# Kernel tuning notes

Measured on AMD Instinct MI355X. Metric: run time of the kernel, lower is better.

## Reference

```python
import jax, jax.numpy as jnp
import numpy as np

THRESH = 0.1        # Huber threshold (self.threshold)
CORR_WT = 1.0       # corr_wt
ENTROPY_WT = 0.0001 # entropy_wt
BS, N = 32, 1024    # n_pts = nv = 1024 hardcoded in multi_pose_with_pts


def setup_inputs() -> dict:
    key = jax.random.key(0)
    ks = jax.random.split(key, 7)
    return {
        "points_1": jax.random.normal(ks[0], (BS, N, 3), jnp.float32),
        "points_2": jax.random.normal(ks[1], (BS, N, 3), jnp.float32),
        "assign_mat_1": jax.random.normal(ks[2], (BS, N, N), jnp.float32),
        "assign_mat_2": jax.random.normal(ks[3], (BS, N, N), jnp.float32),
        "scale": jax.random.uniform(ks[4], (BS,), jnp.float32, 0.5, 1.5),
        "rotation": jax.random.normal(ks[5], (BS, 3, 3), jnp.float32),
        "translation": jax.random.normal(ks[6], (BS, 3), jnp.float32),
    }


def _transform(sRt, pts):
    # apply 4x4 pose to [b, n, 3] points (homogeneous, keep xyz)
    return jnp.einsum('bij,bnj->bni', sRt[:, :3, :3], pts) + sRt[:, :3, 3][:, None, :]


def _chamfer(x, y):
    # squared pairwise distances [b, n, m]; loss = mean min both directions
    d = (jnp.sum(x * x, -1)[:, :, None] + jnp.sum(y * y, -1)[:, None, :]
         - 2.0 * jnp.einsum('bnd,bmd->bnm', x, y))
    d = jnp.maximum(d, 0.0)
    return jnp.mean(jnp.min(d, axis=2)) + jnp.mean(jnp.min(d, axis=1))


def _corr(a, b):
    # smooth-L1-like (Huber) correspondence loss
    diff = jnp.abs(a - b)
    loss = jnp.where(diff > THRESH, diff - THRESH / 2.0, diff * diff / (2.0 * THRESH))
    return CORR_WT * jnp.mean(jnp.sum(loss, axis=2))


def _entropy(assign_mat, soft_assign, axis):
    log_assign = jax.nn.log_softmax(assign_mat, axis=axis)
    return ENTROPY_WT * jnp.mean(-jnp.sum(soft_assign * log_assign, axis=axis))


def _cos_loss(m1, m2, eps=1e-8):
    a = m1.reshape(m1.shape[0], -1)
    b = m2.reshape(m2.shape[0], -1)
    na = jnp.maximum(jnp.linalg.norm(a, axis=1), eps)
    nb = jnp.maximum(jnp.linalg.norm(b, axis=1), eps)
    return jnp.mean(1.0 - jnp.sum(a * b, axis=1) / (na * nb))


def reference(points_1, points_2, assign_mat_1, assign_mat_2, scale, rotation, translation):
    sa1 = jax.nn.softmax(assign_mat_1, axis=2)
    sa2 = jax.nn.softmax(assign_mat_2, axis=2)

    # pose_dict_RT: sRt = [[s*R, t], [0, 1]]
    sR = rotation * scale[:, None, None]
    sRt = jnp.concatenate([sR, translation[:, :, None]], axis=2)          # b 3 4
    bottom = jnp.broadcast_to(jnp.array([0., 0., 0., 1.], sRt.dtype), (sRt.shape[0], 1, 4))
    sRt12 = jnp.concatenate([sRt, bottom], axis=1)                        # b 4 4
    sRt21 = jnp.linalg.inv(sRt12)

    p1in2 = jnp.einsum('bnm,bmd->bnd', sa1, points_2)
    p2in1 = jnp.einsum('bnm,bmd->bnd', sa2, points_1)
    p1to2 = _transform(sRt12, points_1)
    p2to1 = _transform(sRt21, points_2)

    cd1 = _chamfer(p1to2, p1in2)
    cd2 = _chamfer(p2to1, p2in1)
    total = (cd1 + cd2
             + _corr(p1in2, p1to2) + _corr(p2in1, p2to1)
             + _entropy(assign_mat_1, sa1, 2) + _entropy(assign_mat_2, sa2, 2)
             + _cos_loss(assign_mat_1, assign_mat_2)
             + _entropy(assign_mat_1, sa1, 1) + _entropy(assign_mat_2, sa2, 1))
    return total
```

## Files before the change

kernel.cpp:

```cpp
#include <hip/hip_runtime.h>
#include <math.h>

#define BSZ 32
#define NP  1024

#define OFF_ACC   0
#define OFF_COS   8
#define OFF_POSE  104
#define OFF_P1IN2 872
#define OFF_P2IN1 (OFF_P1IN2 + 98304)
#define OFF_INVR  (OFF_P2IN1 + 98304)
#define OFF_COLP  (OFF_INVR + 65536)

__global__ void k_pose(const float* __restrict__ scale,
                       const float* __restrict__ rot,
                       const float* __restrict__ tr,
                       float* __restrict__ ws) {
    int t = threadIdx.x;
    if (t < 52) {
        ws[OFF_ACC + 2 * t]     = 0.f;
        ws[OFF_ACC + 2 * t + 1] = 0.f;
    }
    if (t >= BSZ) return;
    int b = t;
    float s = scale[b];
    float M[9];
#pragma unroll
    for (int i = 0; i < 9; ++i) M[i] = rot[b * 9 + i] * s;
    float t0 = tr[b * 3 + 0], t1 = tr[b * 3 + 1], t2 = tr[b * 3 + 2];
    float det = M[0] * (M[4] * M[8] - M[5] * M[7])
              - M[1] * (M[3] * M[8] - M[5] * M[6])
              + M[2] * (M[3] * M[7] - M[4] * M[6]);
    float id = 1.0f / det;
    float inv[9];
    inv[0] =  (M[4] * M[8] - M[5] * M[7]) * id;
    inv[1] = -(M[1] * M[8] - M[2] * M[7]) * id;
    inv[2] =  (M[1] * M[5] - M[2] * M[4]) * id;
    inv[3] = -(M[3] * M[8] - M[5] * M[6]) * id;
    inv[4] =  (M[0] * M[8] - M[2] * M[6]) * id;
    inv[5] = -(M[0] * M[5] - M[2] * M[3]) * id;
    inv[6] =  (M[3] * M[7] - M[4] * M[6]) * id;
    inv[7] = -(M[0] * M[7] - M[1] * M[6]) * id;
    inv[8] =  (M[0] * M[4] - M[1] * M[3]) * id;
    float u0 = -(inv[0] * t0 + inv[1] * t1 + inv[2] * t2);
    float u1 = -(inv[3] * t0 + inv[4] * t1 + inv[5] * t2);
    float u2 = -(inv[6] * t0 + inv[7] * t1 + inv[8] * t2);
    float* P = ws + OFF_POSE + b * 24;
#pragma unroll
    for (int i = 0; i < 9; ++i) P[i] = M[i];
    P[9] = t0; P[10] = t1; P[11] = t2;
#pragma unroll
    for (int i = 0; i < 9; ++i) P[12 + i] = inv[i];
    P[21] = u0; P[22] = u1; P[23] = u2;
}

__global__ __launch_bounds__(256) void k_rows(
    const float* __restrict__ am1, const float* __restrict__ am2,
    const float* __restrict__ pts1, const float* __restrict__ pts2,
    float* __restrict__ p1in2, float* __restrict__ p2in1,
    float* __restrict__ invR, float* __restrict__ acc) {
    __shared__ float sred[8];
    const int bid = blockIdx.x;
    const int rb = bid & 31;
    const int m  = (bid >> 5) & 1;
    const int b  = bid >> 6;
    const int wv = threadIdx.x >> 6, ln = threadIdx.x & 63;
    const int row0 = rb * 32 + wv * 8;
    const float* am  = m ? am2 : am1;
    const float* pts = m ? pts1 : pts2;
    float* pout   = m ? p2in1 : p1in2;
    float* invout = invR + (m * BSZ + b) * NP;

    float P[16][3];
#pragma unroll
    for (int j = 0; j < 4; ++j)
#pragma unroll
        for (int k = 0; k < 4; ++k) {
            int c = 256 * j + 4 * ln + k;
            const float* p = pts + ((size_t)b * NP + c) * 3;
            P[4 * j + k][0] = p[0];
            P[4 * j + k][1] = p[1];
            P[4 * j + k][2] = p[2];
        }

    float e2a = 0.f, sSa = 0.f;
    const float4* rA = (const float4*)(am + ((size_t)b * NP + row0) * NP);

#pragma unroll 1
    for (int r = 0; r < 8; ++r) {
        float4 a[4];
#pragma unroll
        for (int j = 0; j < 4; ++j) a[j] = rA[(size_t)r * 256 + ln + 64 * j];
        float R = 0.f, Su = 0.f, q0 = 0.f, q1 = 0.f, q2 = 0.f;
#pragma unroll
        for (int j = 0; j < 4; ++j) {
            float* e = (float*)&a[j];
#pragma unroll
            for (int k = 0; k < 4; ++k) {
                int i = 4 * j + k;
                float v  = e[k];
                float ex = __expf(v);
                R += ex; Su += ex * v;
                q0 += ex * P[i][0]; q1 += ex * P[i][1]; q2 += ex * P[i][2];
            }
        }
#pragma unroll
        for (int s = 1; s < 64; s <<= 1) {
            R  += __shfl_xor(R, s);  Su += __shfl_xor(Su, s);
            q0 += __shfl_xor(q0, s); q1 += __shfl_xor(q1, s); q2 += __shfl_xor(q2, s);
        }
        if (ln == 0) {
            float inv = 1.0f / R;
            float S = Su * inv;
            e2a += __logf(R) - S;
            sSa += S;
            int row = row0 + r;
            invout[row] = inv;
            float* o = pout + ((size_t)b * NP + row) * 3;
            o[0] = q0 * inv; o[1] = q1 * inv; o[2] = q2 * inv;
        }
    }
    if (ln == 0) { sred[wv] = e2a; sred[4 + wv] = sSa; }
    __syncthreads();
    if (threadIdx.x == 0) {
        atomicAdd(&acc[0], sred[0] + sred[1] + sred[2] + sred[3]);
        atomicAdd(&acc[1], sred[4] + sred[5] + sred[6] + sred[7]);
    }
}

__global__ __launch_bounds__(256) void k_cols2(
    const float* __restrict__ am1, const float* __restrict__ am2,
    const float* __restrict__ invR, float* __restrict__ colP,
    float* __restrict__ cosacc) {
    __shared__ float invL[64];
    __shared__ float cred[12];
    const int rt = blockIdx.x & 31;
    const int b  = blockIdx.x >> 5;
    const int t  = threadIdx.x;
    if (t < 64) {
        int mm = t >> 5, rr = t & 31;
        invL[t] = invR[(mm * BSZ + b) * NP + rt * 32 + rr];
    }
    __syncthreads();
    const float4* s1 = (const float4*)(am1 + ((size_t)b * NP + rt * 32) * NP) + t;
    const float4* s2 = (const float4*)(am2 + ((size_t)b * NP + rt * 32) * NP) + t;
    float C1x=0,C1y=0,C1z=0,C1w=0, T1x=0,T1y=0,T1z=0,T1w=0;
    float C2x=0,C2y=0,C2z=0,C2w=0, T2x=0,T2y=0,T2z=0,T2w=0;
    float dacc = 0.f, n1a = 0.f, n2a = 0.f;
#pragma unroll 4
    for (int r = 0; r < 32; ++r) {
        float4 v1 = s1[(size_t)r * 256];
        float4 v2 = s2[(size_t)r * 256];
        dacc += v1.x*v2.x + v1.y*v2.y + v1.z*v2.z + v1.w*v2.w;
        n1a  += v1.x*v1.x + v1.y*v1.y + v1.z*v1.z + v1.w*v1.w;
        n2a  += v2.x*v2.x + v2.y*v2.y + v2.z*v2.z + v2.w*v2.w;
        float w1 = invL[r], w2 = invL[32 + r];
        float e;
        e = __expf(v1.x); C1x += e; T1x += e * w1;
        e = __expf(v1.y); C1y += e; T1y += e * w1;
        e = __expf(v1.z); C1z += e; T1z += e * w1;
        e = __expf(v1.w); C1w += e; T1w += e * w1;
        e = __expf(v2.x); C2x += e; T2x += e * w2;
        e = __expf(v2.y); C2y += e; T2y += e * w2;
        e = __expf(v2.z); C2z += e; T2z += e * w2;
        e = __expf(v2.w); C2w += e; T2w += e * w2;
    }
    float4* cp = (float4*)colP + ((size_t)(b * 32 + rt)) * 1024 + t;
    cp[0]   = make_float4(C1x, C1y, C1z, C1w);
    cp[256] = make_float4(T1x, T1y, T1z, T1w);
    cp[512] = make_float4(C2x, C2y, C2z, C2w);
    cp[768] = make_float4(T2x, T2y, T2z, T2w);
#pragma unroll
    for (int s = 1; s < 64; s <<= 1) {
        dacc += __shfl_xor(dacc, s);
        n1a  += __shfl_xor(n1a, s);
        n2a  += __shfl_xor(n2a, s);
    }
    if ((t & 63) == 0) {
        int wv = t >> 6;
        cred[wv] = dacc; cred[4 + wv] = n1a; cred[8 + wv] = n2a;
    }
    __syncthreads();
    if (t == 0) {
        atomicAdd(&cosacc[b],      cred[0] + cred[1] + cred[2]  + cred[3]);
        atomicAdd(&cosacc[32 + b], cred[4] + cred[5] + cred[6]  + cred[7]);
        atomicAdd(&cosacc[64 + b], cred[8] + cred[9] + cred[10] + cred[11]);
    }
}

__global__ void k_colred2(const float* __restrict__ colP, float* __restrict__ acc) {
    int idx = blockIdx.x * 256 + threadIdx.x;
    int bm = idx >> 10;
    int c  = idx & 1023;
    int b = bm >> 1, m = bm & 1;
    const float* base = colP + (size_t)b * 32 * 4 * NP + (2 * m) * NP + c;
    float C = 0.f, T = 0.f;
#pragma unroll
    for (int rt = 0; rt < 32; ++rt) {
        C += base[(size_t)rt * 4 * NP];
        T += base[(size_t)rt * 4 * NP + NP];
    }
    float v = T * __logf(C);
#pragma unroll
    for (int s = 1; s < 64; s <<= 1) v += __shfl_xor(v, s);
    if ((threadIdx.x & 63) == 0) atomicAdd(&acc[2], v);
}

__global__ __launch_bounds__(256) void k_cham(
    const float* __restrict__ p1, const float* __restrict__ p2,
    const float* __restrict__ p1in2, const float* __restrict__ p2in1,
    const float* __restrict__ pose, float* __restrict__ acc) {
    __shared__ float4 ys[NP];
    const int blk   = blockIdx.x;
    const int chunk = blk & 3;
    const int b     = (blk >> 2) & 31;
    const int dir   = (blk >> 7) & 1;
    const int pair  = blk >> 8;
    const float* P   = pose + b * 24 + pair * 12;
    const float* raw = pair ? p2 : p1;
    const float* inA = pair ? p2in1 : p1in2;
    const int t = threadIdx.x;

    float m0 = P[0], m1 = P[1], m2 = P[2];
    float m3 = P[3], m4 = P[4], m5 = P[5];
    float m6 = P[6], m7 = P[7], m8 = P[8];
    float t0 = P[9], t1 = P[10], t2 = P[11];

#pragma unroll
    for (int i = 0; i < 4; ++i) {
        int q = t + 256 * i;
        int gi = (b * NP + q) * 3;
        float x, y, z;
        if (dir == 0) { x = inA[gi]; y = inA[gi + 1]; z = inA[gi + 2]; }
        else {
            float rx = raw[gi], ry = raw[gi + 1], rz = raw[gi + 2];
            x = m0 * rx + m1 * ry + m2 * rz + t0;
            y = m3 * rx + m4 * ry + m5 * rz + t1;
            z = m6 * rx + m7 * ry + m8 * rz + t2;
        }
        ys[q] = make_float4(x, y, z, x * x + y * y + z * z);
    }
    __syncthreads();

    int xi = chunk * 256 + t;
    int gx = (b * NP + xi) * 3;
    float x0, x1, x2;
    if (dir == 0) {
        float rx = raw[gx], ry = raw[gx + 1], rz = raw[gx + 2];
        x0 = m0 * rx + m1 * ry + m2 * rz + t0;
        x1 = m3 * rx + m4 * ry + m5 * rz + t1;
        x2 = m6 * rx + m7 * ry + m8 * rz + t2;
    } else { x0 = inA[gx]; x1 = inA[gx + 1]; x2 = inA[gx + 2]; }
    float sx = x0 * x0 + x1 * x1 + x2 * x2;

    float mn = 3.0e38f;
#pragma unroll 4
    for (int o = 0; o < NP; ++o) {
        float4 yv = ys[o];
        float d = fmaf(-2.0f, x0 * yv.x + x1 * yv.y + x2 * yv.z, sx + yv.w);
        mn = fminf(mn, d);
    }
    mn = fmaxf(mn, 0.0f);

    float v = mn;
#pragma unroll
    for (int m = 1; m < 64; m <<= 1) v += __shfl_xor(v, m);
    if ((t & 63) == 0) atomicAdd(&acc[4], v);

    if (dir == 0) {
        float4 a = ys[xi];
        float s = 0.f;
        float d0 = fabsf(a.x - x0); s += (d0 > 0.1f) ? (d0 - 0.05f) : (d0 * d0 * 5.0f);
        float d1 = fabsf(a.y - x1); s += (d1 > 0.1f) ? (d1 - 0.05f) : (d1 * d1 * 5.0f);
        float d2 = fabsf(a.z - x2); s += (d2 > 0.1f) ? (d2 - 0.05f) : (d2 * d2 * 5.0f);
#pragma unroll
        for (int m = 1; m < 64; m <<= 1) s += __shfl_xor(s, m);
        if ((t & 63) == 0) atomicAdd(&acc[3], s);
    }
}

__global__ void k_final(const float* __restrict__ acc, const float* __restrict__ cosacc,
                        float* __restrict__ out) {
    if (threadIdx.x != 0) return;
    const float invBN = 1.0f / 32768.0f;
    float ent2 = 1e-4f * acc[0] * invBN;
    float ent1 = 1e-4f * (acc[2] - acc[1]) * invBN;
    float corr = acc[3] * invBN;
    float cham = acc[4] * invBN;
    float cosl = 0.f;
    for (int b = 0; b < 32; ++b) {
        float dot = cosacc[b];
        float na = fmaxf(sqrtf(cosacc[32 + b]), 1e-8f);
        float nb = fmaxf(sqrtf(cosacc[64 + b]), 1e-8f);
        cosl += 1.0f - dot / (na * nb);
    }
    cosl *= (1.0f / 32.0f);
    out[0] = cham + corr + ent2 + ent1 + cosl;
}

extern "C" void kernel_launch(void* const* d_in, const int* in_sizes, int n_in,
                              void* d_out, int out_size, void* d_ws, size_t ws_size,
                              hipStream_t stream) {
    const float* p1    = (const float*)d_in[0];
    const float* p2    = (const float*)d_in[1];
    const float* am1   = (const float*)d_in[2];
    const float* am2   = (const float*)d_in[3];
    const float* scale = (const float*)d_in[4];
    const float* rot   = (const float*)d_in[5];
    const float* tr    = (const float*)d_in[6];

    float* ws = (float*)d_ws;
    float* acc    = ws + OFF_ACC;
    float* cosacc = ws + OFF_COS;
    float* pose   = ws + OFF_POSE;
    float* p1in2  = ws + OFF_P1IN2;
    float* p2in1  = ws + OFF_P2IN1;
    float* invR   = ws + OFF_INVR;
    float* colP   = ws + OFF_COLP;

    k_pose<<<1, 64, 0, stream>>>(scale, rot, tr, ws);
    k_rows<<<2048, 256, 0, stream>>>(am1, am2, p1, p2, p1in2, p2in1, invR, acc);
    k_cols2<<<1024, 256, 0, stream>>>(am1, am2, invR, colP, cosacc);
    k_colred2<<<256, 256, 0, stream>>>(colP, acc);
    k_cham<<<512, 256, 0, stream>>>(p1, p2, p1in2, p2in1, pose, acc);
    k_final<<<1, 64, 0, stream>>>(acc, cosacc, (float*)d_out);
}
```

Baseline: 470.9 us.

## Fuse row softmax and column-entropy passes into one kernel over assignment matrices

Merges the row pass and the column pass into a single kernel, so each 1024x1024 assignment matrix is read once instead of twice. Column sums of exp and of the row-normalised probabilities are accumulated per thread and combined through shared-memory atomics into per-block partials. The cosine dot product and norms are folded into the same pass, with the m==0 blocks also reading am2. Points move from registers into shared memory. This adds shared-memory atomics, an extra am2 read in half the blocks, and larger per-block partial buffers.

```diff
diff --git a/kernel.cpp b/kernel.cpp
--- a/kernel.cpp
+++ b/kernel.cpp
@@ -9,8 +9,7 @@
 #define OFF_POSE  104
 #define OFF_P1IN2 872
 #define OFF_P2IN1 (OFF_P1IN2 + 98304)
-#define OFF_INVR  (OFF_P2IN1 + 98304)
-#define OFF_COLP  (OFF_INVR + 65536)
+#define OFF_COLP  (OFF_P2IN1 + 98304)
 
 __global__ void k_pose(const float* __restrict__ scale,
                        const float* __restrict__ rot,
@@ -54,12 +53,14 @@
     P[21] = u0; P[22] = u1; P[23] = u2;
 }
 
-__global__ __launch_bounds__(256) void k_rows(
+__global__ __launch_bounds__(256) void k_main(
     const float* __restrict__ am1, const float* __restrict__ am2,
     const float* __restrict__ pts1, const float* __restrict__ pts2,
     float* __restrict__ p1in2, float* __restrict__ p2in1,
-    float* __restrict__ invR, float* __restrict__ acc) {
-    __shared__ float sred[8];
+    float* __restrict__ colP, float* __restrict__ cosacc, float* __restrict__ acc) {
+    __shared__ float ptsL[3072];
+    __shared__ float cacc[2048];
+    __shared__ float sred[16];
     const int bid = blockIdx.x;
     const int rb = bid & 31;
     const int m  = (bid >> 5) & 1;
@@ -68,29 +69,38 @@
     const int row0 = rb * 32 + wv * 8;
     const float* am  = m ? am2 : am1;
     const float* pts = m ? pts1 : pts2;
-    float* pout   = m ? p2in1 : p1in2;
-    float* invout = invR + (m * BSZ + b) * NP;
-
-    float P[16][3];
-#pragma unroll
-    for (int j = 0; j < 4; ++j)
-#pragma unroll
-        for (int k = 0; k < 4; ++k) {
-            int c = 256 * j + 4 * ln + k;
-            const float* p = pts + ((size_t)b * NP + c) * 3;
-            P[4 * j + k][0] = p[0];
-            P[4 * j + k][1] = p[1];
-            P[4 * j + k][2] = p[2];
-        }
-
-    float e2a = 0.f, sSa = 0.f;
-    const float4* rA = (const float4*)(am + ((size_t)b * NP + row0) * NP);
+    float* pout = m ? p2in1 : p1in2;
+
+    for (int i = threadIdx.x; i < 2048; i += 256) cacc[i] = 0.f;
+    for (int t = threadIdx.x; t < 3072; t += 256) {
+        int c = t / 3, d = t - 3 * c;
+        ptsL[d * 1024 + 256 * (c & 3) + (c >> 2)] = pts[b * 3072 + t];
+    }
+    __syncthreads();
+
+    float C[16], T[16];
+#pragma unroll
+    for (int i = 0; i < 16; ++i) { C[i] = 0.f; T[i] = 0.f; }
+    float e2a = 0.f, sSa = 0.f, dacc = 0.f, na = 0.f;
+
+    const float4* rA = (const float4*)(am  + ((size_t)b * NP + row0) * NP);
+    const float4* rB = (const float4*)(am2 + ((size_t)b * NP + row0) * NP);
 
 #pragma unroll 1
     for (int r = 0; r < 8; ++r) {
         float4 a[4];
 #pragma unroll
         for (int j = 0; j < 4; ++j) a[j] = rA[(size_t)r * 256 + ln + 64 * j];
+#pragma unroll
+        for (int j = 0; j < 4; ++j)
+            na += a[j].x * a[j].x + a[j].y * a[j].y + a[j].z * a[j].z + a[j].w * a[j].w;
+        if (m == 0) {
+#pragma unroll
+            for (int j = 0; j < 4; ++j) {
+                float4 c4 = rB[(size_t)r * 256 + ln + 64 * j];
+                dacc += a[j].x * c4.x + a[j].y * c4.y + a[j].z * c4.z + a[j].w * c4.w;
+            }
+        }
         float R = 0.f, Su = 0.f, q0 = 0.f, q1 = 0.f, q2 = 0.f;
 #pragma unroll
         for (int j = 0; j < 4; ++j) {
@@ -98,10 +108,15 @@
 #pragma unroll
             for (int k = 0; k < 4; ++k) {
                 int i = 4 * j + k;
+                int pidx = 256 * k + 64 * j + ln;
                 float v  = e[k];
                 float ex = __expf(v);
                 R += ex; Su += ex * v;
-                q0 += ex * P[i][0]; q1 += ex * P[i][1]; q2 += ex * P[i][2];
+                q0 += ex * ptsL[pidx];
+                q1 += ex * ptsL[1024 + pidx];
+                q2 += ex * ptsL[2048 + pidx];
+                C[i] += ex;
+                e[k] = ex;
             }
         }
 #pragma unroll
@@ -109,96 +124,64 @@
             R  += __shfl_xor(R, s);  Su += __shfl_xor(Su, s);
             q0 += __shfl_xor(q0, s); q1 += __shfl_xor(q1, s); q2 += __shfl_xor(q2, s);
         }
+        float inv = 1.0f / R;
+#pragma unroll
+        for (int j = 0; j < 4; ++j) {
+            float* e = (float*)&a[j];
+#pragma unroll
+            for (int k = 0; k < 4; ++k) T[4 * j + k] += e[k] * inv;
+        }
+        float S = Su * inv;
         if (ln == 0) {
-            float inv = 1.0f / R;
-            float S = Su * inv;
             e2a += __logf(R) - S;
             sSa += S;
             int row = row0 + r;
-            invout[row] = inv;
             float* o = pout + ((size_t)b * NP + row) * 3;
             o[0] = q0 * inv; o[1] = q1 * inv; o[2] = q2 * inv;
         }
     }
-    if (ln == 0) { sred[wv] = e2a; sred[4 + wv] = sSa; }
+
+#pragma unroll
+    for (int j = 0; j < 4; ++j)
+#pragma unroll
+        for (int k = 0; k < 4; ++k) {
+            int i = 4 * j + k;
+            int c = 256 * j + 4 * ln + k;
+            atomicAdd(&cacc[c],        C[i]);
+            atomicAdd(&cacc[1024 + c], T[i]);
+        }
+#pragma unroll
+    for (int s = 1; s < 64; s <<= 1) {
+        dacc += __shfl_xor(dacc, s);
+        na   += __shfl_xor(na, s);
+    }
+    if (ln == 0) { sred[wv] = e2a; sred[4 + wv] = sSa; sred[8 + wv] = dacc; sred[12 + wv] = na; }
     __syncthreads();
     if (threadIdx.x == 0) {
         atomicAdd(&acc[0], sred[0] + sred[1] + sred[2] + sred[3]);
         atomicAdd(&acc[1], sred[4] + sred[5] + sred[6] + sred[7]);
-    }
-}
-
-__global__ __launch_bounds__(256) void k_cols2(
-    const float* __restrict__ am1, const float* __restrict__ am2,
-    const float* __restrict__ invR, float* __restrict__ colP,
-    float* __restrict__ cosacc) {
-    __shared__ float invL[64];
-    __shared__ float cred[12];
-    const int rt = blockIdx.x & 31;
-    const int b  = blockIdx.x >> 5;
-    const int t  = threadIdx.x;
-    if (t < 64) {
-        int mm = t >> 5, rr = t & 31;
-        invL[t] = invR[(mm * BSZ + b) * NP + rt * 32 + rr];
-    }
-    __syncthreads();
-    const float4* s1 = (const float4*)(am1 + ((size_t)b * NP + rt * 32) * NP) + t;
-    const float4* s2 = (const float4*)(am2 + ((size_t)b * NP + rt * 32) * NP) + t;
-    float C1x=0,C1y=0,C1z=0,C1w=0, T1x=0,T1y=0,T1z=0,T1w=0;
-    float C2x=0,C2y=0,C2z=0,C2w=0, T2x=0,T2y=0,T2z=0,T2w=0;
-    float dacc = 0.f, n1a = 0.f, n2a = 0.f;
-#pragma unroll 4
-    for (int r = 0; r < 32; ++r) {
-        float4 v1 = s1[(size_t)r * 256];
-        float4 v2 = s2[(size_t)r * 256];
-        dacc += v1.x*v2.x + v1.y*v2.y + v1.z*v2.z + v1.w*v2.w;
-        n1a  += v1.x*v1.x + v1.y*v1.y + v1.z*v1.z + v1.w*v1.w;
-        n2a  += v2.x*v2.x + v2.y*v2.y + v2.z*v2.z + v2.w*v2.w;
-        float w1 = invL[r], w2 = invL[32 + r];
-        float e;
-        e = __expf(v1.x); C1x += e; T1x += e * w1;
-        e = __expf(v1.y); C1y += e; T1y += e * w1;
-        e = __expf(v1.z); C1z += e; T1z += e * w1;
-        e = __expf(v1.w); C1w += e; T1w += e * w1;
-        e = __expf(v2.x); C2x += e; T2x += e * w2;
-        e = __expf(v2.y); C2y += e; T2y += e * w2;
-        e = __expf(v2.z); C2z += e; T2z += e * w2;
-        e = __expf(v2.w); C2w += e; T2w += e * w2;
-    }
-    float4* cp = (float4*)colP + ((size_t)(b * 32 + rt)) * 1024 + t;
-    cp[0]   = make_float4(C1x, C1y, C1z, C1w);
-    cp[256] = make_float4(T1x, T1y, T1z, T1w);
-    cp[512] = make_float4(C2x, C2y, C2z, C2w);
-    cp[768] = make_float4(T2x, T2y, T2z, T2w);
-#pragma unroll
-    for (int s = 1; s < 64; s <<= 1) {
-        dacc += __shfl_xor(dacc, s);
-        n1a  += __shfl_xor(n1a, s);
-        n2a  += __shfl_xor(n2a, s);
-    }
-    if ((t & 63) == 0) {
-        int wv = t >> 6;
-        cred[wv] = dacc; cred[4 + wv] = n1a; cred[8 + wv] = n2a;
-    }
-    __syncthreads();
-    if (t == 0) {
-        atomicAdd(&cosacc[b],      cred[0] + cred[1] + cred[2]  + cred[3]);
-        atomicAdd(&cosacc[32 + b], cred[4] + cred[5] + cred[6]  + cred[7]);
-        atomicAdd(&cosacc[64 + b], cred[8] + cred[9] + cred[10] + cred[11]);
-    }
-}
-
-__global__ void k_colred2(const float* __restrict__ colP, float* __restrict__ acc) {
+        if (m == 0) {
+            atomicAdd(&cosacc[b],      sred[8]  + sred[9]  + sred[10] + sred[11]);
+            atomicAdd(&cosacc[32 + b], sred[12] + sred[13] + sred[14] + sred[15]);
+        } else {
+            atomicAdd(&cosacc[64 + b], sred[12] + sred[13] + sred[14] + sred[15]);
+        }
+    }
+    float4* cp = (float4*)(colP + (size_t)bid * 2048);
+    const float4* cs = (const float4*)cacc;
+    for (int i = threadIdx.x; i < 512; i += 256) cp[i] = cs[i];
+}
+
+__global__ void k_colred(const float* __restrict__ colP, float* __restrict__ acc) {
     int idx = blockIdx.x * 256 + threadIdx.x;
     int bm = idx >> 10;
     int c  = idx & 1023;
-    int b = bm >> 1, m = bm & 1;
-    const float* base = colP + (size_t)b * 32 * 4 * NP + (2 * m) * NP + c;
+    const float* base = colP + (size_t)bm * 32 * 2048 + c;
     float C = 0.f, T = 0.f;
 #pragma unroll
-    for (int rt = 0; rt < 32; ++rt) {
-        C += base[(size_t)rt * 4 * NP];
-        T += base[(size_t)rt * 4 * NP + NP];
+    for (int rbi = 0; rbi < 32; ++rbi) {
+        C += base[(size_t)rbi * 2048];
+        T += base[(size_t)rbi * 2048 + 1024];
     }
     float v = T * __logf(C);
 #pragma unroll
@@ -315,13 +298,11 @@
     float* pose   = ws + OFF_POSE;
     float* p1in2  = ws + OFF_P1IN2;
     float* p2in1  = ws + OFF_P2IN1;
-    float* invR   = ws + OFF_INVR;
     float* colP   = ws + OFF_COLP;
 
     k_pose<<<1, 64, 0, stream>>>(scale, rot, tr, ws);
-    k_rows<<<2048, 256, 0, stream>>>(am1, am2, p1, p2, p1in2, p2in1, invR, acc);
-    k_cols2<<<1024, 256, 0, stream>>>(am1, am2, invR, colP, cosacc);
-    k_colred2<<<256, 256, 0, stream>>>(colP, acc);
+    k_main<<<2048, 256, 0, stream>>>(am1, am2, p1, p2, p1in2, p2in1, colP, cosacc, acc);
+    k_colred<<<256, 256, 0, stream>>>(colP, acc);
     k_cham<<<512, 256, 0, stream>>>(p1, p2, p1in2, p2in1, pose, acc);
     k_final<<<1, 64, 0, stream>>>(acc, cosacc, (float*)d_out);
 }
```

Result: slower. 484.5 us (+2.9%).
